# Optimization experiments

Measured on AMD Instinct MI355X. Metric: run time of the kernel, lower is better.

The kernel has to match this reference:

```python
import jax, jax.numpy as jnp
import numpy as np


def group_norm(x, g, b, groups, eps=1e-5):
    # x: (B, C, H, W), PyTorch GroupNorm semantics
    B, C, H, W = x.shape
    xr = x.reshape(B, groups, -1)
    m = xr.mean(-1, keepdims=True)
    v = xr.var(-1, keepdims=True)
    xn = ((xr - m) * jax.lax.rsqrt(v + eps)).reshape(B, C, H, W)
    return xn * g[:, None, None] + b[:, None, None]


def mamba(xs, in_w, conv_w, conv_b, xproj_w, dt_w, dt_b, A_log, D, out_w):
    # Standard Mamba block: in_proj -> causal depthwise conv -> SiLU ->
    # x_proj -> softplus(dt_proj) -> selective scan -> gate -> out_proj.
    Bsz, L, d = xs.shape
    di = in_w.shape[0] // 2
    r = dt_w.shape[1]
    n = A_log.shape[1]
    K = conv_w.shape[1]
    xz = xs @ in_w.T                           # (B, L, 2*di)
    xpart, z = xz[..., :di], xz[..., di:]
    xp = jnp.pad(xpart, ((0, 0), (K - 1, 0), (0, 0)))  # causal pad
    xc = conv_b + sum(xp[:, k:k + L, :] * conv_w[:, k] for k in range(K))
    xc = jax.nn.silu(xc)
    proj = xc @ xproj_w.T                      # (B, L, r + 2n)
    dt = proj[..., :r]
    Bm = proj[..., r:r + n]
    Cm = proj[..., r + n:]
    delta = jax.nn.softplus(dt @ dt_w.T + dt_b)   # (B, L, di)
    A = -jnp.exp(A_log)                            # (di, n)
    dA = jnp.exp(jnp.einsum('bld,dn->bldn', delta, A))
    dBu = jnp.einsum('bld,bln,bld->bldn', delta, Bm, xc)

    def step(h, inp):
        dA_t, dBu_t, C_t = inp
        h = dA_t * h + dBu_t                  # (B, di, n)
        return h, jnp.einsum('bdn,bn->bd', h, C_t)

    h0 = jnp.zeros((Bsz, di, n), xs.dtype)
    _, ys = jax.lax.scan(step, h0, (jnp.moveaxis(dA, 1, 0), jnp.moveaxis(dBu, 1, 0), jnp.moveaxis(Cm, 1, 0)))
    y = jnp.moveaxis(ys, 0, 1) + D * xc
    y = y * jax.nn.silu(z)
    return y @ out_w.T


def setup_inputs() -> dict:
    def nrm(i, shape, s=0.05):
        return jax.random.normal(jax.random.fold_in(jax.random.key(0), i), shape, dtype=jnp.float32) * s

    f32 = jnp.float32
    C = 128
    di, r, n = 256, 8, 16          # spa mamba: d_model=128, expand=2
    di2, r2 = 64, 2                # spe mamba: d_model=32
    A1 = jnp.log(jnp.broadcast_to(jnp.arange(1, n + 1, dtype=f32), (di, n)))
    A2 = jnp.log(jnp.broadcast_to(jnp.arange(1, n + 1, dtype=f32), (di2, n)))
    return {
        'x': nrm(0, (2, C, 64, 64), 1.0),
        'pe_w': nrm(1, (C, C)), 'pe_b': jnp.zeros((C,), f32),
        'pe_gn_g': jnp.ones((C,), f32), 'pe_gn_b': jnp.zeros((C,), f32),
        'spa_in_w': nrm(2, (2 * di, C)),
        'spa_conv_w': nrm(3, (di, 4)), 'spa_conv_b': jnp.zeros((di,), f32),
        'spa_xproj_w': nrm(4, (r + 2 * n, di)),
        'spa_dt_w': nrm(5, (di, r)), 'spa_dt_b': jnp.full((di,), -2.0, f32),
        'spa_Alog': A1, 'spa_D': jnp.ones((di,), f32),
        'spa_out_w': nrm(6, (C, di)),
        'spa_gn_g': jnp.ones((C,), f32), 'spa_gn_b': jnp.zeros((C,), f32),
        'spe_in_w': nrm(7, (2 * di2, 32)),
        'spe_conv_w': nrm(8, (di2, 4)), 'spe_conv_b': jnp.zeros((di2,), f32),
        'spe_xproj_w': nrm(9, (r2 + 2 * n, di2)),
        'spe_dt_w': nrm(10, (di2, r2)), 'spe_dt_b': jnp.full((di2,), -2.0, f32),
        'spe_Alog': A2, 'spe_D': jnp.ones((di2,), f32),
        'spe_out_w': nrm(11, (32, di2)),
        'spe_gn_g': jnp.ones((C,), f32), 'spe_gn_b': jnp.zeros((C,), f32),
        'fuse_w': jnp.full((2,), 0.5, f32),
        'cls_w': nrm(12, (10, C)), 'cls_b': jnp.zeros((10,), f32),
        'ref_dw_w': nrm(13, (C, 1, 3, 3)),
        'ref_gn_g': jnp.ones((C,), f32), 'ref_gn_b': jnp.zeros((C,), f32),
        'ref_pw_w': nrm(14, (1, C)), 'ref_pw_b': jnp.zeros((1,), f32),
        'alpha': jnp.asarray(1e-4, f32),
    }


def reference(x, pe_w, pe_b, pe_gn_g, pe_gn_b, spa_in_w, spa_conv_w, spa_conv_b, spa_xproj_w, spa_dt_w, spa_dt_b, spa_Alog, spa_D, spa_out_w, spa_gn_g, spa_gn_b, spe_in_w, spe_conv_w, spe_conv_b, spe_xproj_w, spe_dt_w, spe_dt_b, spe_Alog, spe_D, spe_out_w, spe_gn_g, spe_gn_b, fuse_w, cls_w, cls_b, ref_dw_w, ref_gn_g, ref_gn_b, ref_pw_w, ref_pw_b, alpha):
    B, _, H, W = x.shape
    # patch embedding: 1x1 conv + GroupNorm + SiLU
    h1 = jnp.einsum('bchw,oc->bohw', x, pe_w) + pe_b[:, None, None]
    h1 = jax.nn.silu(group_norm(h1, pe_gn_g, pe_gn_b, 4))
    # SpaMamba: scan over flattened spatial tokens (B, H*W, C)
    seq = h1.transpose(0, 2, 3, 1).reshape(B, H * W, -1)
    y = mamba(seq, spa_in_w, spa_conv_w, spa_conv_b, spa_xproj_w, spa_dt_w, spa_dt_b, spa_Alog, spa_D, spa_out_w)
    y = y.reshape(B, H, W, -1).transpose(0, 3, 1, 2)
    spa = jax.nn.silu(group_norm(y, spa_gn_g, spa_gn_b, 4)) + h1
    # SpeMamba: token_num=4, group_channel_num=32, channel_num=128 (no pad)
    seq2 = h1.transpose(0, 2, 3, 1).reshape(B * H * W, 4, 32)
    y2 = mamba(seq2, spe_in_w, spe_conv_w, spe_conv_b, spe_xproj_w, spe_dt_w, spe_dt_b, spe_Alog, spe_D, spe_out_w)
    y2 = y2.reshape(B, H, W, -1).transpose(0, 3, 1, 2)
    spe = h1 + jax.nn.silu(group_norm(y2, spe_gn_g, spe_gn_b, 4))
    # attention-weighted fusion + residual (BothMamba, use_att=True)
    wts = jax.nn.softmax(fuse_w)
    feat = spa * wts[0] + spe * wts[1] + h1
    # classifier head (1x1 conv)
    logits = jnp.einsum('bchw,oc->bohw', feat, cls_w) + cls_b[:, None, None]
    # BoundaryAwareLogitRefiner
    edge = jax.lax.conv_general_dilated(feat, ref_dw_w, (1, 1), ((1, 1), (1, 1)), feature_group_count=feat.shape[1], dimension_numbers=('NCHW', 'OIHW', 'NCHW'))
    edge = jax.nn.silu(group_norm(edge, ref_gn_g, ref_gn_b, 4))
    edge = jax.nn.sigmoid(jnp.einsum('bchw,oc->bohw', edge, ref_pw_w) + ref_pw_b[:, None, None])
    local = jax.lax.reduce_window(logits, 0.0, jax.lax.add, (1, 1, 3, 3), (1, 1, 1, 1), ((0, 0), (0, 0), (1, 1), (1, 1))) / 9.0  # count_include_pad=True
    return logits + alpha * (1.0 - edge) * (local - logits)
```

## Files before the change

### kernel.cpp

```cpp
#include <hip/hip_runtime.h>
#include <math.h>

#define DEV __device__ __forceinline__

DEV float sigm(float x){ return 1.f/(1.f+__expf(-x)); }
DEV float siluf(float x){ return x * sigm(x); }
DEV float softplusf(float x){ return x > 20.f ? x : log1pf(__expf(x)); }

static constexpr float NG = 131072.0f;
static constexpr float LOG2E = 1.4426950408889634f;

static constexpr size_t WS_H1    = 0;
static constexpr size_t WS_H1PRE = 1048576;
static constexpr size_t WS_XC    = 2097152;
static constexpr size_t WS_ZSIL  = 4194304;
static constexpr size_t WS_XZ    = 6291456;
static constexpr size_t WS_QOFF  = 6619136;
static constexpr size_t WS_LOG   = 8650752;
static constexpr size_t WS_Y     = 10485760;
static constexpr size_t WS_POFF  = 12582912;
static constexpr size_t WS_Y2    = 14155776;
static constexpr size_t WS_FEAT  = 15204352;
static constexpr size_t WS_STATS = 16252928;

__global__ void __launch_bounds__(256)
k_red(const float* __restrict__ part, float* __restrict__ outS, int half){
  __shared__ float red[4];
  int b = blockIdx.x >> 3, j = blockIdx.x & 7;
  float s = 0.f;
  for (int i = b*half + threadIdx.x; i < (b+1)*half; i += 256)
    s += part[(size_t)i*8 + j];
  s += __shfl_xor(s,1); s += __shfl_xor(s,2); s += __shfl_xor(s,4);
  s += __shfl_xor(s,8); s += __shfl_xor(s,16); s += __shfl_xor(s,32);
  if ((threadIdx.x & 63) == 0) red[threadIdx.x>>6] = s;
  __syncthreads();
  if (threadIdx.x == 0) outS[b*8+j] = red[0]+red[1]+red[2]+red[3];
}

__global__ void __launch_bounds__(256)
k_pe(const float* __restrict__ x, const float* __restrict__ pe_w,
     const float* __restrict__ pe_b, float* __restrict__ h1pre,
     float* __restrict__ part){
  __shared__ float As[16][36];
  __shared__ float Bs[16][64];
  __shared__ float red1[2][4], red2[2][4];
  int tid = threadIdx.x;
  int nx = blockIdx.x, my = blockIdx.y;
  int m0 = my*32, n0 = nx*64;
  int b = m0 >> 12, pl0 = m0 & 4095;
  int tx = tid & 15, ty = tid >> 4;
  float acc[2][4];
  #pragma unroll
  for (int i = 0; i < 2; i++)
    #pragma unroll
    for (int j = 0; j < 4; j++) acc[i][j] = 0.f;
  for (int k0 = 0; k0 < 128; k0 += 16){
    if (tid < 128){
      int k = tid >> 3, mm = (tid & 7)*4;
      float4 a = *(const float4*)(x + ((size_t)b*128 + k0+k)*4096 + pl0 + mm);
      *(float4*)&As[k][mm] = a;
    }
    {
      int n = tid >> 2, kq = (tid & 3)*4;
      float4 a = *(const float4*)(pe_w + (size_t)(n0+n)*128 + k0 + kq);
      Bs[kq+0][n] = a.x; Bs[kq+1][n] = a.y; Bs[kq+2][n] = a.z; Bs[kq+3][n] = a.w;
// ... 21 lines not shown
  }
  s1 += __shfl_xor(s1,1);  s2 += __shfl_xor(s2,1);
  s1 += __shfl_xor(s1,2);  s2 += __shfl_xor(s2,2);
  s1 += __shfl_xor(s1,4);  s2 += __shfl_xor(s2,4);
  s1 += __shfl_xor(s1,16); s2 += __shfl_xor(s2,16);
  s1 += __shfl_xor(s1,32); s2 += __shfl_xor(s2,32);
  int lane = tid & 63, w = tid >> 6;
  if ((lane & 55) == 0){
    int gl = (lane >> 3) & 1;
    red1[gl][w] = s1; red2[gl][w] = s2;
  }
  __syncthreads();
  if (tid < 8){
    int gg = tid >> 1, which = tid & 1;
    int gl = gg - nx*2;
    float v = 0.f;
    if (gl == 0 || gl == 1){
      v = which ? (red2[gl][0]+red2[gl][1]+red2[gl][2]+red2[gl][3])
                : (red1[gl][0]+red1[gl][1]+red1[gl][2]+red1[gl][3]);
    }
    int pblk = b*256 + (my & 127)*2 + nx;
    part[(size_t)pblk*8 + tid] = v;
  }
}

__global__ void __launch_bounds__(256)
k_xz(const float* __restrict__ h1pre, const float* __restrict__ in_w,
     const float* __restrict__ stats, const float* __restrict__ gng,
     const float* __restrict__ gnb, float* __restrict__ h1,
     float* __restrict__ xz, float* __restrict__ zsil){
  __shared__ float As[16][68];
  __shared__ float Bs[16][64];
  int tid = threadIdx.x;
  int m0 = blockIdx.y*64, n0 = blockIdx.x*64;
  int tx = tid & 15, ty = tid >> 4;
  float acc[4][4];
  #pragma unroll
  for (int i = 0; i < 4; i++)
    #pragma unroll
    for (int j = 0; j < 4; j++) acc[i][j] = 0.f;
  for (int k0 = 0; k0 < 128; k0 += 16){
    {
      int m = tid >> 2, kk = (tid & 3)*4;
      int pixm = m0 + m, c0 = k0 + kk;
      int bb = pixm >> 12, g = c0 >> 5;
      float4 a = *(const float4*)(h1pre + (size_t)pixm*128 + c0);
// ... 89 lines not shown
  {
    int t = tid & 15, jq = tid >> 4;
    int tok = m0 + t;
    float a0 = 0.f, a1 = 0.f, a2 = 0.f;
    for (int k0 = 0; k0 < 256; k0 += 4){
      float4 av = *(const float4*)&xct[t*260 + k0];
      float4 w0 = *(const float4*)(xpw + (size_t)jq*256 + k0);
      float4 w1 = *(const float4*)(xpw + (size_t)(jq+16)*256 + k0);
      a0 += av.x*w0.x + av.y*w0.y + av.z*w0.z + av.w*w0.w;
      a1 += av.x*w1.x + av.y*w1.y + av.z*w1.z + av.w*w1.w;
      if (jq < 8){
        float4 w2 = *(const float4*)(xpw + (size_t)(jq+32)*256 + k0);
        a2 += av.x*w2.x + av.y*w2.y + av.z*w2.z + av.w*w2.w;
      }
    }
    float* pr = proj + (size_t)tok*40;
    pr[jq] = a0;
    pr[jq+16] = a1;
    if (jq < 8) pr[jq+32] = a2;
  }
}

__global__ void __launch_bounds__(256)
k_delta(const float* __restrict__ proj, const float* __restrict__ dtw,
        const float* __restrict__ dtb, float* __restrict__ delta){
  int tid = threadIdx.x;
  int tok = blockIdx.x*4 + (tid >> 6);
  int lane = tid & 63;
  int d0 = lane*4;
  const float4* pr4 = (const float4*)(proj + (size_t)tok*40);
  float4 p0 = pr4[0], p1 = pr4[1];
  float4 outv;
  float* po = (float*)&outv;
  #pragma unroll
  for (int j = 0; j < 4; j++){
    int d = d0 + j;
    const float4* wr = (const float4*)(dtw + (size_t)d*8);
    float4 w0 = wr[0], w1 = wr[1];
    float v = dtb[d] + p0.x*w0.x + p0.y*w0.y + p0.z*w0.z + p0.w*w0.w
                     + p1.x*w1.x + p1.y*w1.y + p1.z*w1.z + p1.w*w1.w;
    po[j] = softplusf(v);
  }
  *(float4*)(delta + (size_t)tok*256 + d0) = outv;
}

__global__ void __launch_bounds__(256)
k_scan1(const float* __restrict__ delta, const float* __restrict__ proj,
        const float* __restrict__ xc, const float* __restrict__ Alog,
        float* __restrict__ P, float* __restrict__ Q){
  int blk = blockIdx.x;
  int dblk = blk & 3;
  int bc = blk >> 2;
  int b = bc >> 8, chunk = bc & 255;
  int tid = threadIdx.x;
  int dl = tid >> 2, ng = tid & 3;
  int d = dblk*64 + dl;
  float4 a4 = *(const float4*)(Alog + (size_t)d*16 + ng*4);
  float An[4] = {-__expf(a4.x)*LOG2E, -__expf(a4.y)*LOG2E,
                 -__expf(a4.z)*LOG2E, -__expf(a4.w)*LOG2E};
  float Pv[4] = {1.f,1.f,1.f,1.f}, Qv[4] = {0.f,0.f,0.f,0.f};
  size_t row0 = (size_t)(b*4096 + chunk*16);
  for (int l = 0; l < 16; l++){
    size_t r = row0 + l;
    float dv = delta[r*256 + d];
    float xv = xc[r*256 + d];
    float4 bm = *(const float4*)(proj + r*40 + 8 + ng*4);
    float dBx = dv*xv;
    float bmv[4] = {bm.x, bm.y, bm.z, bm.w};
    #pragma unroll
    for (int k = 0; k < 4; k++){
      float a = exp2f(dv*An[k]);
      Qv[k] = a*Qv[k] + bmv[k]*dBx;
      Pv[k] *= a;
    }
  }
  size_t o = (size_t)bc*4096 + dblk*1024 + tid*4;
  float4 pv; pv.x=Pv[0]; pv.y=Pv[1]; pv.z=Pv[2]; pv.w=Pv[3];
  float4 qv; qv.x=Qv[0]; qv.y=Qv[1]; qv.z=Qv[2]; qv.w=Qv[3];
  *(float4*)(P + o) = pv;
  *(float4*)(Q + o) = qv;
}

__global__ void __launch_bounds__(256)
k_scan2(const float* __restrict__ P, const float* __restrict__ Q,
        float* __restrict__ hs){
  __shared__ float Ps[256][17], Qs[256][17];
  int tid = threadIdx.x;
// ... 26 lines not shown
      if (lane >= off){ q = p*qp + q; p = p*pp; }
    }
    float h0 = __shfl_up(q, 1);
    if (lane == 0) h0 = 0.f;
    float h1 = p0*h0 + q0;
    float h2 = p1*h1 + q1;
    float h3 = p2*h2 + q2;
    Ps[4*lane+0][c] = h0;
    Ps[4*lane+1][c] = h1;
    Ps[4*lane+2][c] = h2;
    Ps[4*lane+3][c] = h3;
  }
  __syncthreads();
  for (int i = tid; i < 1024; i += 256){
    int ch = i >> 2, g = (i & 3)*4;
    size_t gaddr = (size_t)(b*256+ch)*4096 + dn0 + g;
    float4 h;
    h.x = Ps[ch][g]; h.y = Ps[ch][g+1]; h.z = Ps[ch][g+2]; h.w = Ps[ch][g+3];
    *(float4*)(hs + gaddr) = h;
  }
}

__global__ void __launch_bounds__(256)
k_scan3(const float* __restrict__ delta, const float* __restrict__ proj,
        const float* __restrict__ xc, const float* __restrict__ zsil,
        const float* __restrict__ Alog, const float* __restrict__ Dv,
        const float* __restrict__ hs, float* __restrict__ y){
  int blk = blockIdx.x;
  int dblk = blk & 3;
  int bc = blk >> 2;
  int b = bc >> 8, chunk = bc & 255;
  int tid = threadIdx.x;
  int dl = tid >> 2, ng = tid & 3;
  int d = dblk*64 + dl;
  float4 a4 = *(const float4*)(Alog + (size_t)d*16 + ng*4);
  float An[4] = {-__expf(a4.x)*LOG2E, -__expf(a4.y)*LOG2E,
                 -__expf(a4.z)*LOG2E, -__expf(a4.w)*LOG2E};
  float Dd = Dv[d];
  float h[4];
  {
    size_t o = (size_t)bc*4096 + dblk*1024 + tid*4;
    float4 hv = *(const float4*)(hs + o);
    h[0]=hv.x; h[1]=hv.y; h[2]=hv.z; h[3]=hv.w;
  }
  size_t row0 = (size_t)(b*4096 + chunk*16);
  for (int l = 0; l < 16; l++){
    size_t r = row0 + l;
    float dv = delta[r*256 + d];
    float xv = xc[r*256 + d];
    float4 bm = *(const float4*)(proj + r*40 + 8 + ng*4);
    float4 cm = *(const float4*)(proj + r*40 + 24 + ng*4);
    float dBx = dv*xv;
    float bmv[4] = {bm.x, bm.y, bm.z, bm.w};
    float cmv[4] = {cm.x, cm.y, cm.z, cm.w};
    float ys = 0.f;
    #pragma unroll
    for (int k = 0; k < 4; k++){
      float a = exp2f(dv*An[k]);
      h[k] = a*h[k] + bmv[k]*dBx;
      ys += h[k]*cmv[k];
    }
    ys += __shfl_xor(ys, 1);
    ys += __shfl_xor(ys, 2);
    if (ng == 0){
      float zv = zsil[r*256 + d];
      y[r*256 + d] = (ys + Dd*xv) * zv;
    }
  }
}

__global__ void __launch_bounds__(256)
k_outproj(const float* __restrict__ y, const float* __restrict__ out_w,
          float* __restrict__ yproj, float* __restrict__ part){
  __shared__ float As[16][36];
  __shared__ float Bs[16][64];
  __shared__ float red1[2][4], red2[2][4];
  int tid = threadIdx.x;
  int nx = blockIdx.x, my = blockIdx.y;
  int m0 = my*32, n0 = nx*64;
  int b = m0 >> 12;
  int tx = tid & 15, ty = tid >> 4;
  float acc[2][4];
  #pragma unroll
  for (int i = 0; i < 2; i++)
    #pragma unroll
    for (int j = 0; j < 4; j++) acc[i][j] = 0.f;
  for (int k0 = 0; k0 < 256; k0 += 16){
    if (tid < 128){
      int m = tid >> 2, kk = (tid & 3)*4;
      float4 a = *(const float4*)(y + (size_t)(m0+m)*256 + k0+kk);
      As[kk+0][m] = a.x; As[kk+1][m] = a.y; As[kk+2][m] = a.z; As[kk+3][m] = a.w;
    }
    {
      int n = tid >> 2, kq = (tid & 3)*4;
      float4 a = *(const float4*)(out_w + (size_t)(n0+n)*256 + k0 + kq);
      Bs[kq+0][n] = a.x; Bs[kq+1][n] = a.y; Bs[kq+2][n] = a.z; Bs[kq+3][n] = a.w;
// ... 18 lines not shown
  }
  s1 += __shfl_xor(s1,1);  s2 += __shfl_xor(s2,1);
  s1 += __shfl_xor(s1,2);  s2 += __shfl_xor(s2,2);
  s1 += __shfl_xor(s1,4);  s2 += __shfl_xor(s2,4);
  s1 += __shfl_xor(s1,16); s2 += __shfl_xor(s2,16);
  s1 += __shfl_xor(s1,32); s2 += __shfl_xor(s2,32);
  int lane = tid & 63, w = tid >> 6;
  if ((lane & 55) == 0){
    int gl = (lane >> 3) & 1;
    red1[gl][w] = s1; red2[gl][w] = s2;
  }
  __syncthreads();
  if (tid < 8){
    int gg = tid >> 1, which = tid & 1;
    int gl = gg - nx*2;
    float v = 0.f;
    if (gl == 0 || gl == 1){
      v = which ? (red2[gl][0]+red2[gl][1]+red2[gl][2]+red2[gl][3])
                : (red1[gl][0]+red1[gl][1]+red1[gl][2]+red1[gl][3]);
    }
    int pblk = b*256 + (my & 127)*2 + nx;
    part[(size_t)pblk*8 + tid] = v;
  }
}

__global__ void __launch_bounds__(256)
k_spe_a(const float* __restrict__ h1, const float* __restrict__ in_w,
        const float* __restrict__ conv_w, const float* __restrict__ conv_b,
        float* __restrict__ xc2, float* __restrict__ xc2T,
        float* __restrict__ zsil2){
  __shared__ float s_in[4][128];
  int tid = threadIdx.x;
  int w = tid >> 6, lane = tid & 63;
  float wx[32], wz[32];
  {
    const float4* rx = (const float4*)(in_w + (size_t)lane*32);
    const float4* rz = (const float4*)(in_w + (size_t)(64+lane)*32);
    #pragma unroll
    for (int k = 0; k < 8; k++){
      float4 a = rx[k]; wx[k*4]=a.x; wx[k*4+1]=a.y; wx[k*4+2]=a.z; wx[k*4+3]=a.w;
      float4 b = rz[k]; wz[k*4]=b.x; wz[k*4+1]=b.y; wz[k*4+2]=b.z; wz[k*4+3]=b.w;
    }
  }
  float4 cwv = ((const float4*)conv_w)[lane];
  float cbv = conv_b[lane];
  for (int i = 0; i < 4; i++){
    int pix = blockIdx.x*16 + w*4 + i;
    float2 hv = ((const float2*)(h1 + (size_t)pix*128))[lane];
    s_in[w][2*lane] = hv.x; s_in[w][2*lane+1] = hv.y;
    float xpr[4], zs[4];
    #pragma unroll
    for (int l = 0; l < 4; l++){
      const float4* sv = (const float4*)&s_in[w][l*32];
      float ax = 0.f, az = 0.f;
      #pragma unroll
      for (int c4 = 0; c4 < 8; c4++){
        float4 v = sv[c4];
        ax += v.x*wx[c4*4] + v.y*wx[c4*4+1] + v.z*wx[c4*4+2] + v.w*wx[c4*4+3];
        az += v.x*wz[c4*4] + v.y*wz[c4*4+1] + v.z*wz[c4*4+2] + v.w*wz[c4*4+3];
      }
      xpr[l] = ax; zs[l] = siluf(az);
    }
    #pragma unroll
    for (int l = 0; l < 4; l++){
      float v = cbv;
      if (l >= 3) v += xpr[l-3]*cwv.x;
      if (l >= 2) v += xpr[l-2]*cwv.y;
      if (l >= 1) v += xpr[l-1]*cwv.z;
      v += xpr[l]*cwv.w;
      float sx = siluf(v);
      int tok = pix*4 + l;
      xc2 [(size_t)tok*64 + lane] = sx;
      xc2T[(size_t)lane*32768 + tok] = sx;
      zsil2[(size_t)tok*64 + lane] = zs[l];
    }
  }
}

__global__ void __launch_bounds__(256)
k_spe_b(const float* __restrict__ xc2T, const float* __restrict__ xpw,
        float* __restrict__ proj){
  int tok = blockIdx.x*256 + threadIdx.x;
  float xcv[64];
  #pragma unroll 64
  for (int dd = 0; dd < 64; dd++) xcv[dd] = xc2T[(size_t)dd*32768 + tok];
  float* pr = proj + (size_t)tok*36;
  #pragma unroll 2
  for (int j = 0; j < 34; j++){
    const float4* wr = (const float4*)(xpw + j*64);
    float a = 0.f;
    #pragma unroll
    for (int k = 0; k < 16; k++){
      float4 wv = wr[k];
      a += xcv[k*4]*wv.x + xcv[k*4+1]*wv.y + xcv[k*4+2]*wv.z + xcv[k*4+3]*wv.w;
    }
    pr[j] = a;
  }
}

__global__ void __launch_bounds__(256)
k_spe_c(const float* __restrict__ xc2, const float* __restrict__ zsil2,
        const float* __restrict__ proj, const float* __restrict__ dt_w,
        const float* __restrict__ dt_b, const float* __restrict__ Alog,
        const float* __restrict__ Dvec, float* __restrict__ yg){
  int tid = threadIdx.x;
  int w = tid >> 6, lane = tid & 63;
  float2 dtwv = ((const float2*)dt_w)[lane];
  float dbv = dt_b[lane], Dd = Dvec[lane];
  float An[16];
  {
    const float4* ar = (const float4*)(Alog + (size_t)lane*16);
    #pragma unroll
    for (int k = 0; k < 4; k++){
      float4 a = ar[k];
      An[k*4]   = -__expf(a.x)*LOG2E; An[k*4+1] = -__expf(a.y)*LOG2E;
      An[k*4+2] = -__expf(a.z)*LOG2E; An[k*4+3] = -__expf(a.w)*LOG2E;
    }
  }
  for (int i = 0; i < 4; i++){
    int pix = blockIdx.x*16 + w*4 + i;
    float h[16];
    #pragma unroll
    for (int n = 0; n < 16; n++) h[n] = 0.f;
    #pragma unroll
    for (int l = 0; l < 4; l++){
      int tok = pix*4 + l;
      float pj[36];
      {
        const float4* pr = (const float4*)(proj + (size_t)tok*36);
        #pragma unroll
        for (int k = 0; k < 9; k++){
          float4 v = pr[k];
          pj[k*4]=v.x; pj[k*4+1]=v.y; pj[k*4+2]=v.z; pj[k*4+3]=v.w;
        }
      }
      float xv = xc2[(size_t)tok*64 + lane];
      float zv = zsil2[(size_t)tok*64 + lane];
      float dt = softplusf(dbv + pj[0]*dtwv.x + pj[1]*dtwv.y);
      float ys = 0.f;
      #pragma unroll
      for (int n = 0; n < 16; n++){
        float a = exp2f(dt * An[n]);
        h[n] = a*h[n] + dt * pj[2+n] * xv;
        ys += h[n] * pj[18+n];
      }
      yg[(size_t)tok*64 + lane] = (ys + Dd*xv) * zv;
    }
  }
}

__global__ void __launch_bounds__(256)
k_spe_d(const float* __restrict__ yg, const float* __restrict__ out_w,
        float* __restrict__ y2, float* __restrict__ part){
  __shared__ float ldsWT[64*32];
  __shared__ float bst[8];
  int tid = threadIdx.x;
  for (int i = tid; i < 2048; i += 256){
    int c2 = i >> 6, dd = i & 63;
    ldsWT[dd*32 + c2] = out_w[i];
  }
  if (tid < 8) bst[tid] = 0.f;
  __syncthreads();
  int w = tid >> 6, lane = tid & 63;
  int c2 = lane & 31, slot = lane >> 5;
  int tokbase = blockIdx.x*64 + w*16 + slot;
  float acc[8];
  #pragma unroll
  for (int i = 0; i < 8; i++) acc[i] = 0.f;
  for (int dd4 = 0; dd4 < 16; dd4++){
    float w0 = ldsWT[(dd4*4+0)*32 + c2];
    float w1 = ldsWT[(dd4*4+1)*32 + c2];
    float w2 = ldsWT[(dd4*4+2)*32 + c2];
    float w3 = ldsWT[(dd4*4+3)*32 + c2];
    #pragma unroll
    for (int i = 0; i < 8; i++){
      int tok = tokbase + 2*i;
      float4 yv = ((const float4*)(yg + (size_t)tok*64))[dd4];
      acc[i] += yv.x*w0 + yv.y*w1 + yv.z*w2 + yv.w*w3;
    }
  }
  #pragma unroll
  for (int i = 0; i < 8; i++){
    int tok = tokbase + 2*i;
    int pix = tok >> 2, l = tok & 3;
    y2[(size_t)pix*128 + l*32 + c2] = acc[i];
    float s1 = acc[i], s2 = acc[i]*acc[i];
    s1 += __shfl_xor(s1,1);  s2 += __shfl_xor(s2,1);
    s1 += __shfl_xor(s1,2);  s2 += __shfl_xor(s2,2);
    s1 += __shfl_xor(s1,4);  s2 += __shfl_xor(s2,4);
    s1 += __shfl_xor(s1,8);  s2 += __shfl_xor(s2,8);
    s1 += __shfl_xor(s1,16); s2 += __shfl_xor(s2,16);
    if (c2 == 0){
      atomicAdd(&bst[l*2+0], s1);
      atomicAdd(&bst[l*2+1], s2);
    }
  }
  __syncthreads();
  if (tid < 8) part[(size_t)blockIdx.x*8 + tid] = bst[tid];
}

__global__ void __launch_bounds__(256)
k_fuse(const float* __restrict__ h1, const float* __restrict__ yproj,
       const float* __restrict__ y2, const float* __restrict__ stats,
       const float* __restrict__ spa_g, const float* __restrict__ spa_b,
       const float* __restrict__ spe_g, const float* __restrict__ spe_b,
       const float* __restrict__ fuse_w, const float* __restrict__ cls_w,
       const float* __restrict__ cls_b, float* __restrict__ feat,
       float* __restrict__ logits){
  __shared__ float ft[2][128];
  int tid = threadIdx.x;
  int pixl = tid >> 7, c = tid & 127;
  int pix = blockIdx.x*2 + pixl;
  int b = pix >> 12, g = c >> 5;
  float m1 = stats[16 + (b*4+g)*2]   * (1.f/NG);
  float v1 = stats[16 + (b*4+g)*2+1] * (1.f/NG) - m1*m1;
  float m2 = stats[32 + (b*4+g)*2]   * (1.f/NG);
  float v2 = stats[32 + (b*4+g)*2+1] * (1.f/NG) - m2*m2;
  float h = h1[(size_t)pix*128 + c];
  float sa = siluf((yproj[(size_t)pix*128+c] - m1)*rsqrtf(v1+1e-5f)*spa_g[c] + spa_b[c]) + h;
  float sp = h + siluf((y2[(size_t)pix*128+c] - m2)*rsqrtf(v2+1e-5f)*spe_g[c] + spe_b[c]);
  float e0 = __expf(fuse_w[0]), e1 = __expf(fuse_w[1]);
  float w0 = e0/(e0+e1), w1 = e1/(e0+e1);
  float f = sa*w0 + sp*w1 + h;
  feat[(size_t)pix*128+c] = f;
  ft[pixl][c] = f;
  __syncthreads();
  if (tid < 20){
    int pl = (tid >= 10) ? 1 : 0;
    int o = tid - pl*10;
    float acc = cls_b[o];
    for (int cc = 0; cc < 128; cc++) acc += ft[pl][cc]*cls_w[o*128+cc];
    logits[(size_t)(blockIdx.x*2 + pl)*16 + o] = acc;
  }
}

__global__ void __launch_bounds__(256)
k_dw(const float* __restrict__ feat, const float* __restrict__ dww,
     float* __restrict__ epre, float* __restrict__ part){
  __shared__ float ft[100*128];
  __shared__ float red1[4][64], red2[4][64];
  int tid = threadIdx.x;
  int blk = blockIdx.x;
  int b = blk >> 6, ty = (blk >> 3) & 7, tx = blk & 7;
  for (int idx = tid; idx < 100*128; idx += 256){
    int row = idx >> 7, c = idx & 127;
    int r10 = row / 10, c10 = row - r10*10;
    int ry = ty*8 + r10 - 1, rx = tx*8 + c10 - 1;
    float v = 0.f;
    if (ry >= 0 && ry < 64 && rx >= 0 && rx < 64)
      v = feat[(size_t)((b<<12)|(ry<<6)|rx)*128 + c];
    ft[idx] = v;
  }
  __syncthreads();
  int c = tid & 127, pl = tid >> 7;
  float w[9];
  #pragma unroll
  for (int k = 0; k < 9; k++) w[k] = dww[c*9+k];
  float s1 = 0.f, s2 = 0.f;
  for (int i = 0; i < 32; i++){
    int pixl = i*2 + pl;
    int py = pixl >> 3, px = pixl & 7;
    float acc = 0.f;
    #pragma unroll
    for (int dy = 0; dy < 3; dy++)
      #pragma unroll
      for (int dx = 0; dx < 3; dx++)
        acc += ft[((py+dy)*10 + (px+dx))*128 + c] * w[dy*3+dx];
    epre[(size_t)((b<<12)|((ty*8+py)<<6)|(tx*8+px))*128 + c] = acc;
    s1 += acc; s2 += acc*acc;
  }
  int g = c >> 5;
  int idx = (c & 31) | (pl << 5);
  red1[g][idx] = s1; red2[g][idx] = s2;
  __syncthreads();
  int rg = tid >> 6, ridx = tid & 63;
  for (int s = 32; s >= 1; s >>= 1){
    if (ridx < s){ red1[rg][ridx] += red1[rg][ridx+s]; red2[rg][ridx] += red2[rg][ridx+s]; }
    __syncthreads();
  }
  if (ridx == 0){
    part[(size_t)blk*8 + rg*2+0] = red1[rg][0];
    part[(size_t)blk*8 + rg*2+1] = red2[rg][0];
  }
}

__global__ void __launch_bounds__(256)
k_final(const float* __restrict__ epre, const float* __restrict__ logits,
        const float* __restrict__ stats, const float* __restrict__ rg_g,
        const float* __restrict__ rg_b, const float* __restrict__ pw_w,
        const float* __restrict__ pw_b, const float* __restrict__ alpha,
        float* __restrict__ outp){
  __shared__ float part[4];
  __shared__ float edge_s[2];
  int tid = threadIdx.x;
  int pixl = tid >> 7, c = tid & 127;
  int pix = blockIdx.x*2 + pixl;
  int b = pix >> 12, p = pix & 4095, yy = p >> 6, xx = p & 63;
  int g = c >> 5;
  float m = stats[48 + (b*4+g)*2]   * (1.f/NG);
  float v = stats[48 + (b*4+g)*2+1] * (1.f/NG) - m*m;
  float e = epre[(size_t)pix*128+c];
  float en = siluf((e-m)*rsqrtf(v+1e-5f)*rg_g[c] + rg_b[c]);
  float pv = en * pw_w[c];
  pv += __shfl_xor(pv,1);  pv += __shfl_xor(pv,2);  pv += __shfl_xor(pv,4);
  pv += __shfl_xor(pv,8);  pv += __shfl_xor(pv,16); pv += __shfl_xor(pv,32);
  if ((tid & 63) == 0) part[tid>>6] = pv;
// ... 42 lines not shown
  const float* spe_xproj_w= (const float*)d_in[19];
  const float* spe_dt_w   = (const float*)d_in[20];
  const float* spe_dt_b   = (const float*)d_in[21];
  const float* spe_Alog   = (const float*)d_in[22];
  const float* spe_D      = (const float*)d_in[23];
  const float* spe_out_w  = (const float*)d_in[24];
  const float* spe_gn_g   = (const float*)d_in[25];
  const float* spe_gn_b   = (const float*)d_in[26];
  const float* fuse_w     = (const float*)d_in[27];
  const float* cls_w      = (const float*)d_in[28];
  const float* cls_b      = (const float*)d_in[29];
  const float* ref_dw_w   = (const float*)d_in[30];
  const float* ref_gn_g   = (const float*)d_in[31];
  const float* ref_gn_b   = (const float*)d_in[32];
  const float* ref_pw_w   = (const float*)d_in[33];
  const float* ref_pw_b   = (const float*)d_in[34];
  const float* alpha      = (const float*)d_in[35];
  float* ws  = (float*)d_ws;
  float* out = (float*)d_out;

  float* Pb    = ws + WS_POFF;
  float* Qb    = ws + WS_QOFF;
  float* HSb   = Pb;
  float* dely  = ws + WS_Y;
  float* partPE  = ws + WS_Y;
  float* partSPA = ws + WS_POFF;
  float* partSPE = ws + WS_POFF + 16384;
  float* partDW  = ws + WS_POFF + 65536;
  float* proj  = ws + WS_FEAT;
  float* xc2   = ws + WS_XC;
  float* xc2T  = ws + WS_ZSIL;
  float* zsil2 = ws + WS_XZ;
  float* proj2 = ws + WS_XZ + 2097152;
  float* yg    = ws + WS_Y;

  k_pe<<<dim3(2,256),256,0,stream>>>(x, pe_w, pe_b, ws+WS_H1PRE, partPE);
  k_red<<<16,256,0,stream>>>(partPE, ws+WS_STATS+0, 256);
  k_xz<<<dim3(8,128),256,0,stream>>>(ws+WS_H1PRE, spa_in_w, ws+WS_STATS,
      pe_gn_g, pe_gn_b, ws+WS_H1, ws+WS_XZ, ws+WS_ZSIL);
  k_projc<<<512,256,0,stream>>>(ws+WS_XZ, spa_conv_w, spa_conv_b, spa_xproj_w,
      ws+WS_XC, proj);
  k_delta<<<2048,256,0,stream>>>(proj, spa_dt_w, spa_dt_b, dely);
  k_scan1<<<2048,256,0,stream>>>(dely, proj, ws+WS_XC, spa_Alog, Pb, Qb);
  k_scan2<<<512,256,0,stream>>>(Pb, Qb, HSb);
  k_scan3<<<2048,256,0,stream>>>(dely, proj, ws+WS_XC, ws+WS_ZSIL,
      spa_Alog, spa_D, HSb, dely);
  k_outproj<<<dim3(2,256),256,0,stream>>>(dely, spa_out_w, ws+WS_H1PRE, partSPA);
  k_red<<<16,256,0,stream>>>(partSPA, ws+WS_STATS+16, 256);
  k_spe_a<<<512,256,0,stream>>>(ws+WS_H1, spe_in_w, spe_conv_w, spe_conv_b,
      xc2, xc2T, zsil2);
  k_spe_b<<<128,256,0,stream>>>(xc2T, spe_xproj_w, proj2);
  k_spe_c<<<512,256,0,stream>>>(xc2, zsil2, proj2, spe_dt_w, spe_dt_b,
      spe_Alog, spe_D, yg);
  k_spe_d<<<512,256,0,stream>>>(yg, spe_out_w, ws+WS_Y2, partSPE);
  k_red<<<16,256,0,stream>>>(partSPE, ws+WS_STATS+32, 256);
  k_fuse<<<4096,256,0,stream>>>(ws+WS_H1, ws+WS_H1PRE, ws+WS_Y2, ws+WS_STATS,
      spa_gn_g, spa_gn_b, spe_gn_g, spe_gn_b, fuse_w, cls_w, cls_b,
      ws+WS_FEAT, ws+WS_LOG);
  k_dw<<<128,256,0,stream>>>(ws+WS_FEAT, ref_dw_w, ws+WS_Y, partDW);
  k_red<<<16,256,0,stream>>>(partDW, ws+WS_STATS+48, 64);
  k_final<<<4096,256,0,stream>>>(ws+WS_Y, ws+WS_LOG, ws+WS_STATS,
      ref_gn_g, ref_gn_b, ref_pw_w, ref_pw_b, alpha, out);
  (void)in_sizes; (void)n_in; (void)out_size; (void)ws_size;
}
```

Before: 384.1 us.

## Fuse stat reductions via last-block, inline delta into scans, merge spectral Mamba kernels

Replaces the separate k_red launches with a last-block-done reduction using an atomic counter in each stats-producing kernel. It also folds the dt projection and softplus into scan1/scan3 instead of materialising delta. The four spectral Mamba kernels become one kernel that keeps xc, proj and y in LDS. This cuts kernel launches and global round-trips of intermediates, at the cost of recomputing delta in both scan passes, more LDS per block, and an extra memset plus atomic fences.

Measured after the change: 529.0 us. 1.38x slower.

```diff
diff --git a/kernel.cpp b/kernel.cpp
--- a/kernel.cpp
+++ b/kernel.cpp
@@ -22,25 +22,33 @@
 static constexpr size_t WS_Y2    = 14155776;
 static constexpr size_t WS_FEAT  = 15204352;
 static constexpr size_t WS_STATS = 16252928;
-
-__global__ void __launch_bounds__(256)
-k_red(const float* __restrict__ part, float* __restrict__ outS, int half){
-  __shared__ float red[4];
-  int b = blockIdx.x >> 3, j = blockIdx.x & 7;
+static constexpr size_t WS_CNT   = 16252992;
+
+DEV void stats_lastblock(const float* part, int rowsPerB, int gridBlocks,
+                         int* cnt, float* statsOut){
+  __shared__ int lastS;
+  int tid = threadIdx.x;
+  __threadfence();
+  __syncthreads();
+  if (tid == 0) lastS = (atomicAdd(cnt, 1) == gridBlocks - 1) ? 1 : 0;
+  __syncthreads();
+  if (!lastS) return;
+  __threadfence();
+  int p = tid >> 4, sl = tid & 15;
+  int b = p >> 3, j = p & 7;
   float s = 0.f;
-  for (int i = b*half + threadIdx.x; i < (b+1)*half; i += 256)
-    s += part[(size_t)i*8 + j];
-  s += __shfl_xor(s,1); s += __shfl_xor(s,2); s += __shfl_xor(s,4);
-  s += __shfl_xor(s,8); s += __shfl_xor(s,16); s += __shfl_xor(s,32);
-  if ((threadIdx.x & 63) == 0) red[threadIdx.x>>6] = s;
-  __syncthreads();
-  if (threadIdx.x == 0) outS[b*8+j] = red[0]+red[1]+red[2]+red[3];
+  volatile const float* vp = (volatile const float*)part;
+  for (int row = sl; row < rowsPerB; row += 16)
+    s += vp[((size_t)b*rowsPerB + row)*8 + j];
+  s += __shfl_xor(s,1); s += __shfl_xor(s,2);
+  s += __shfl_xor(s,4); s += __shfl_xor(s,8);
+  if (sl == 0) statsOut[p] = s;
 }
 
 __global__ void __launch_bounds__(256)
 k_pe(const float* __restrict__ x, const float* __restrict__ pe_w,
      const float* __restrict__ pe_b, float* __restrict__ h1pre,
-     float* __restrict__ part){
+     float* __restrict__ part, int* __restrict__ cnt, float* __restrict__ statsOut){
   __shared__ float As[16][36];
   __shared__ float Bs[16][64];
   __shared__ float red1[2][4], red2[2][4];
@@ -108,6 +116,7 @@
     int pblk = b*256 + (my & 127)*2 + nx;
     part[(size_t)pblk*8 + tid] = v;
   }
+  stats_lastblock(part, 256, 512, cnt, statsOut);
 }
 
 __global__ void __launch_bounds__(256)
@@ -243,32 +252,10 @@
 }
 
 __global__ void __launch_bounds__(256)
-k_delta(const float* __restrict__ proj, const float* __restrict__ dtw,
-        const float* __restrict__ dtb, float* __restrict__ delta){
-  int tid = threadIdx.x;
-  int tok = blockIdx.x*4 + (tid >> 6);
-  int lane = tid & 63;
-  int d0 = lane*4;
-  const float4* pr4 = (const float4*)(proj + (size_t)tok*40);
-  float4 p0 = pr4[0], p1 = pr4[1];
-  float4 outv;
-  float* po = (float*)&outv;
-  #pragma unroll
-  for (int j = 0; j < 4; j++){
-    int d = d0 + j;
-    const float4* wr = (const float4*)(dtw + (size_t)d*8);
-    float4 w0 = wr[0], w1 = wr[1];
-    float v = dtb[d] + p0.x*w0.x + p0.y*w0.y + p0.z*w0.z + p0.w*w0.w
-                     + p1.x*w1.x + p1.y*w1.y + p1.z*w1.z + p1.w*w1.w;
-    po[j] = softplusf(v);
-  }
-  *(float4*)(delta + (size_t)tok*256 + d0) = outv;
-}
-
-__global__ void __launch_bounds__(256)
-k_scan1(const float* __restrict__ delta, const float* __restrict__ proj,
-        const float* __restrict__ xc, const float* __restrict__ Alog,
-        float* __restrict__ P, float* __restrict__ Q){
+k_scan1(const float* __restrict__ proj, const float* __restrict__ xc,
+        const float* __restrict__ dtw, const float* __restrict__ dtb,
+        const float* __restrict__ Alog, float* __restrict__ P,
+        float* __restrict__ Q){
   int blk = blockIdx.x;
   int dblk = blk & 3;
   int bc = blk >> 2;
@@ -279,11 +266,17 @@
   float4 a4 = *(const float4*)(Alog + (size_t)d*16 + ng*4);
   float An[4] = {-__expf(a4.x)*LOG2E, -__expf(a4.y)*LOG2E,
                  -__expf(a4.z)*LOG2E, -__expf(a4.w)*LOG2E};
+  const float4* wr = (const float4*)(dtw + (size_t)d*8);
+  float4 w0 = wr[0], w1 = wr[1];
+  float bd = dtb[d];
   float Pv[4] = {1.f,1.f,1.f,1.f}, Qv[4] = {0.f,0.f,0.f,0.f};
   size_t row0 = (size_t)(b*4096 + chunk*16);
   for (int l = 0; l < 16; l++){
     size_t r = row0 + l;
-    float dv = delta[r*256 + d];
+    const float4* pr4 = (const float4*)(proj + r*40);
+    float4 p0 = pr4[0], p1 = pr4[1];
+    float dv = softplusf(bd + p0.x*w0.x + p0.y*w0.y + p0.z*w0.z + p0.w*w0.w
+                            + p1.x*w1.x + p1.y*w1.y + p1.z*w1.z + p1.w*w1.w);
     float xv = xc[r*256 + d];
     float4 bm = *(const float4*)(proj + r*40 + 8 + ng*4);
     float dBx = dv*xv;
@@ -356,10 +349,11 @@
 }
 
 __global__ void __launch_bounds__(256)
-k_scan3(const float* __restrict__ delta, const float* __restrict__ proj,
-        const float* __restrict__ xc, const float* __restrict__ zsil,
-        const float* __restrict__ Alog, const float* __restrict__ Dv,
-        const float* __restrict__ hs, float* __restrict__ y){
+k_scan3(const float* __restrict__ proj, const float* __restrict__ xc,
+        const float* __restrict__ zsil, const float* __restrict__ dtw,
+        const float* __restrict__ dtb, const float* __restrict__ Alog,
+        const float* __restrict__ Dv, const float* __restrict__ hs,
+        float* __restrict__ y){
   int blk = blockIdx.x;
   int dblk = blk & 3;
   int bc = blk >> 2;
@@ -370,6 +364,9 @@
   float4 a4 = *(const float4*)(Alog + (size_t)d*16 + ng*4);
   float An[4] = {-__expf(a4.x)*LOG2E, -__expf(a4.y)*LOG2E,
                  -__expf(a4.z)*LOG2E, -__expf(a4.w)*LOG2E};
+  const float4* wr = (const float4*)(dtw + (size_t)d*8);
+  float4 w0 = wr[0], w1 = wr[1];
+  float bd = dtb[d];
   float Dd = Dv[d];
   float h[4];
   {
@@ -380,7 +377,10 @@
   size_t row0 = (size_t)(b*4096 + chunk*16);
   for (int l = 0; l < 16; l++){
     size_t r = row0 + l;
-    float dv = delta[r*256 + d];
+    const float4* pr4 = (const float4*)(proj + r*40);
+    float4 p0 = pr4[0], p1 = pr4[1];
+    float dv = softplusf(bd + p0.x*w0.x + p0.y*w0.y + p0.z*w0.z + p0.w*w0.w
+                            + p1.x*w1.x + p1.y*w1.y + p1.z*w1.z + p1.w*w1.w);
     float xv = xc[r*256 + d];
     float4 bm = *(const float4*)(proj + r*40 + 8 + ng*4);
     float4 cm = *(const float4*)(proj + r*40 + 24 + ng*4);
@@ -405,7 +405,8 @@
 
 __global__ void __launch_bounds__(256)
 k_outproj(const float* __restrict__ y, const float* __restrict__ out_w,
-          float* __restrict__ yproj, float* __restrict__ part){
+          float* __restrict__ yproj, float* __restrict__ part,
+          int* __restrict__ cnt, float* __restrict__ statsOut){
   __shared__ float As[16][36];
   __shared__ float Bs[16][64];
   __shared__ float red1[2][4], red2[2][4];
@@ -470,18 +471,27 @@
     int pblk = b*256 + (my & 127)*2 + nx;
     part[(size_t)pblk*8 + tid] = v;
   }
-}
-
-__global__ void __launch_bounds__(256)
-k_spe_a(const float* __restrict__ h1, const float* __restrict__ in_w,
-        const float* __restrict__ conv_w, const float* __restrict__ conv_b,
-        float* __restrict__ xc2, float* __restrict__ xc2T,
-        float* __restrict__ zsil2){
+  stats_lastblock(part, 256, 512, cnt, statsOut);
+}
+
+__global__ void __launch_bounds__(256)
+k_spe(const float* __restrict__ h1, const float* __restrict__ in_w,
+      const float* __restrict__ conv_w, const float* __restrict__ conv_b,
+      const float* __restrict__ xpw, const float* __restrict__ dt_w,
+      const float* __restrict__ dt_b, const float* __restrict__ Alog,
+      const float* __restrict__ Dvec, const float* __restrict__ out_w,
+      float* __restrict__ y2, float* __restrict__ part,
+      int* __restrict__ cnt, float* __restrict__ statsOut){
+  __shared__ float s_xc[64][66];
+  __shared__ float s_pr[64][37];
   __shared__ float s_in[4][128];
+  __shared__ float bst[8];
   int tid = threadIdx.x;
   int w = tid >> 6, lane = tid & 63;
-  float wx[32], wz[32];
+  if (tid < 8) bst[tid] = 0.f;
+  float xcr[4][4], zsr[4][4];
   {
+    float wx[32], wz[32];
     const float4* rx = (const float4*)(in_w + (size_t)lane*32);
     const float4* rz = (const float4*)(in_w + (size_t)(64+lane)*32);
     #pragma unroll
@@ -489,74 +499,64 @@
       float4 a = rx[k]; wx[k*4]=a.x; wx[k*4+1]=a.y; wx[k*4+2]=a.z; wx[k*4+3]=a.w;
       float4 b = rz[k]; wz[k*4]=b.x; wz[k*4+1]=b.y; wz[k*4+2]=b.z; wz[k*4+3]=b.w;
     }
-  }
-  float4 cwv = ((const float4*)conv_w)[lane];
-  float cbv = conv_b[lane];
-  for (int i = 0; i < 4; i++){
-    int pix = blockIdx.x*16 + w*4 + i;
-    float2 hv = ((const float2*)(h1 + (size_t)pix*128))[lane];
-    s_in[w][2*lane] = hv.x; s_in[w][2*lane+1] = hv.y;
-    float xpr[4], zs[4];
-    #pragma unroll
-    for (int l = 0; l < 4; l++){
-      const float4* sv = (const float4*)&s_in[w][l*32];
-      float ax = 0.f, az = 0.f;
+    float4 cwv = ((const float4*)conv_w)[lane];
+    float cbv = conv_b[lane];
+    #pragma unroll
+    for (int i = 0; i < 4; i++){
+      int pix = blockIdx.x*16 + w*4 + i;
+      float2 hv = ((const float2*)(h1 + (size_t)pix*128))[lane];
+      s_in[w][2*lane] = hv.x; s_in[w][2*lane+1] = hv.y;
+      float xpr[4];
       #pragma unroll
-      for (int c4 = 0; c4 < 8; c4++){
-        float4 v = sv[c4];
-        ax += v.x*wx[c4*4] + v.y*wx[c4*4+1] + v.z*wx[c4*4+2] + v.w*wx[c4*4+3];
-        az += v.x*wz[c4*4] + v.y*wz[c4*4+1] + v.z*wz[c4*4+2] + v.w*wz[c4*4+3];
+      for (int l = 0; l < 4; l++){
+        const float4* sv = (const float4*)&s_in[w][l*32];
+        float ax = 0.f, az = 0.f;
+        #pragma unroll
+        for (int c4 = 0; c4 < 8; c4++){
+          float4 v = sv[c4];
+          ax += v.x*wx[c4*4] + v.y*wx[c4*4+1] + v.z*wx[c4*4+2] + v.w*wx[c4*4+3];
+          az += v.x*wz[c4*4] + v.y*wz[c4*4+1] + v.z*wz[c4*4+2] + v.w*wz[c4*4+3];
+        }
+        xpr[l] = ax; zsr[i][l] = siluf(az);
       }
-      xpr[l] = ax; zs[l] = siluf(az);
-    }
-    #pragma unroll
-    for (int l = 0; l < 4; l++){
-      float v = cbv;
-      if (l >= 3) v += xpr[l-3]*cwv.x;
-      if (l >= 2) v += xpr[l-2]*cwv.y;
-      if (l >= 1) v += xpr[l-1]*cwv.z;
-      v += xpr[l]*cwv.w;
-      float sx = siluf(v);
-      int tok = pix*4 + l;
-      xc2 [(size_t)tok*64 + lane] = sx;
-      xc2T[(size_t)lane*32768 + tok] = sx;
-      zsil2[(size_t)tok*64 + lane] = zs[l];
-    }
-  }
-}
-
-__global__ void __launch_bounds__(256)
-k_spe_b(const float* __restrict__ xc2T, const float* __restrict__ xpw,
-        float* __restrict__ proj){
-  int tok = blockIdx.x*256 + threadIdx.x;
-  float xcv[64];
-  #pragma unroll 64
-  for (int dd = 0; dd < 64; dd++) xcv[dd] = xc2T[(size_t)dd*32768 + tok];
-  float* pr = proj + (size_t)tok*36;
-  #pragma unroll 2
-  for (int j = 0; j < 34; j++){
-    const float4* wr = (const float4*)(xpw + j*64);
-    float a = 0.f;
-    #pragma unroll
-    for (int k = 0; k < 16; k++){
-      float4 wv = wr[k];
-      a += xcv[k*4]*wv.x + xcv[k*4+1]*wv.y + xcv[k*4+2]*wv.z + xcv[k*4+3]*wv.w;
-    }
-    pr[j] = a;
-  }
-}
-
-__global__ void __launch_bounds__(256)
-k_spe_c(const float* __restrict__ xc2, const float* __restrict__ zsil2,
-        const float* __restrict__ proj, const float* __restrict__ dt_w,
-        const float* __restrict__ dt_b, const float* __restrict__ Alog,
-        const float* __restrict__ Dvec, float* __restrict__ yg){
-  int tid = threadIdx.x;
-  int w = tid >> 6, lane = tid & 63;
-  float2 dtwv = ((const float2*)dt_w)[lane];
-  float dbv = dt_b[lane], Dd = Dvec[lane];
-  float An[16];
+      #pragma unroll
+      for (int l = 0; l < 4; l++){
+        float v = cbv;
+        if (l >= 3) v += xpr[l-3]*cwv.x;
+        if (l >= 2) v += xpr[l-2]*cwv.y;
+        if (l >= 1) v += xpr[l-1]*cwv.z;
+        v += xpr[l]*cwv.w;
+        float sx = siluf(v);
+        xcr[i][l] = sx;
+        s_xc[(w*4+i)*4 + l][lane] = sx;
+      }
+    }
+  }
+  __syncthreads();
   {
+    int t = lane;
+    float a[9];
+    #pragma unroll
+    for (int j = 0; j < 9; j++) a[j] = 0.f;
+    for (int k = 0; k < 64; k++){
+      float xk = s_xc[t][k];
+      #pragma unroll
+      for (int j = 0; j < 9; j++){
+        int ja = w*9 + j; if (ja > 33) ja = 33;
+        a[j] += xk * xpw[(size_t)ja*64 + k];
+      }
+    }
+    #pragma unroll
+    for (int j = 0; j < 9; j++){
+      int ja = w*9 + j;
+      if (ja < 34) s_pr[t][ja] = a[j];
+    }
+  }
+  __syncthreads();
+  {
+    float2 dtwv = ((const float2*)dt_w)[lane];
+    float dbv = dt_b[lane], Dd = Dvec[lane];
+    float An[16];
     const float4* ar = (const float4*)(Alog + (size_t)lane*16);
     #pragma unroll
     for (int k = 0; k < 4; k++){
@@ -564,87 +564,61 @@
       An[k*4]   = -__expf(a.x)*LOG2E; An[k*4+1] = -__expf(a.y)*LOG2E;
       An[k*4+2] = -__expf(a.z)*LOG2E; An[k*4+3] = -__expf(a.w)*LOG2E;
     }
-  }
-  for (int i = 0; i < 4; i++){
-    int pix = blockIdx.x*16 + w*4 + i;
-    float h[16];
-    #pragma unroll
-    for (int n = 0; n < 16; n++) h[n] = 0.f;
-    #pragma unroll
-    for (int l = 0; l < 4; l++){
-      int tok = pix*4 + l;
-      float pj[36];
-      {
-        const float4* pr = (const float4*)(proj + (size_t)tok*36);
+    #pragma unroll
+    for (int i = 0; i < 4; i++){
+      float h[16];
+      #pragma unroll
+      for (int n = 0; n < 16; n++) h[n] = 0.f;
+      #pragma unroll
+      for (int l = 0; l < 4; l++){
+        int t = (w*4+i)*4 + l;
+        float dt = softplusf(dbv + s_pr[t][0]*dtwv.x + s_pr[t][1]*dtwv.y);
+        float xv = xcr[i][l], zv = zsr[i][l];
+        float ys = 0.f;
         #pragma unroll
-        for (int k = 0; k < 9; k++){
-          float4 v = pr[k];
-          pj[k*4]=v.x; pj[k*4+1]=v.y; pj[k*4+2]=v.z; pj[k*4+3]=v.w;
+        for (int n = 0; n < 16; n++){
+          float a = exp2f(dt * An[n]);
+          h[n] = a*h[n] + dt * s_pr[t][2+n] * xv;
+          ys += h[n] * s_pr[t][18+n];
         }
+        s_xc[t][lane] = (ys + Dd*xv) * zv;
       }
-      float xv = xc2[(size_t)tok*64 + lane];
-      float zv = zsil2[(size_t)tok*64 + lane];
-      float dt = softplusf(dbv + pj[0]*dtwv.x + pj[1]*dtwv.y);
-      float ys = 0.f;
+    }
+  }
+  __syncthreads();
+  {
+    int t = lane, cg = w;
+    float acc[8];
+    #pragma unroll
+    for (int q = 0; q < 8; q++) acc[q] = 0.f;
+    for (int dd = 0; dd < 64; dd++){
+      float yv = s_xc[t][dd];
       #pragma unroll
-      for (int n = 0; n < 16; n++){
-        float a = exp2f(dt * An[n]);
-        h[n] = a*h[n] + dt * pj[2+n] * xv;
-        ys += h[n] * pj[18+n];
-      }
-      yg[(size_t)tok*64 + lane] = (ys + Dd*xv) * zv;
-    }
-  }
-}
-
-__global__ void __launch_bounds__(256)
-k_spe_d(const float* __restrict__ yg, const float* __restrict__ out_w,
-        float* __restrict__ y2, float* __restrict__ part){
-  __shared__ float ldsWT[64*32];
-  __shared__ float bst[8];
-  int tid = threadIdx.x;
-  for (int i = tid; i < 2048; i += 256){
-    int c2 = i >> 6, dd = i & 63;
-    ldsWT[dd*32 + c2] = out_w[i];
-  }
-  if (tid < 8) bst[tid] = 0.f;
-  __syncthreads();
-  int w = tid >> 6, lane = tid & 63;
-  int c2 = lane & 31, slot = lane >> 5;
-  int tokbase = blockIdx.x*64 + w*16 + slot;
-  float acc[8];
-  #pragma unroll
-  for (int i = 0; i < 8; i++) acc[i] = 0.f;
-  for (int dd4 = 0; dd4 < 16; dd4++){
-    float w0 = ldsWT[(dd4*4+0)*32 + c2];
-    float w1 = ldsWT[(dd4*4+1)*32 + c2];
-    float w2 = ldsWT[(dd4*4+2)*32 + c2];
-    float w3 = ldsWT[(dd4*4+3)*32 + c2];
-    #pragma unroll
-    for (int i = 0; i < 8; i++){
-      int tok = tokbase + 2*i;
-      float4 yv = ((const float4*)(yg + (size_t)tok*64))[dd4];
-      acc[i] += yv.x*w0 + yv.y*w1 + yv.z*w2 + yv.w*w3;
-    }
-  }
-  #pragma unroll
-  for (int i = 0; i < 8; i++){
-    int tok = tokbase + 2*i;
+      for (int q = 0; q < 8; q++)
+        acc[q] += yv * out_w[(size_t)(cg*8+q)*64 + dd];
+    }
+    int tok = blockIdx.x*64 + t;
     int pix = tok >> 2, l = tok & 3;
-    y2[(size_t)pix*128 + l*32 + c2] = acc[i];
-    float s1 = acc[i], s2 = acc[i]*acc[i];
-    s1 += __shfl_xor(s1,1);  s2 += __shfl_xor(s2,1);
-    s1 += __shfl_xor(s1,2);  s2 += __shfl_xor(s2,2);
+    float4 o0, o1;
+    o0.x=acc[0]; o0.y=acc[1]; o0.z=acc[2]; o0.w=acc[3];
+    o1.x=acc[4]; o1.y=acc[5]; o1.z=acc[6]; o1.w=acc[7];
+    *(float4*)(y2 + (size_t)pix*128 + l*32 + cg*8)     = o0;
+    *(float4*)(y2 + (size_t)pix*128 + l*32 + cg*8 + 4) = o1;
+    float s1 = 0.f, s2 = 0.f;
+    #pragma unroll
+    for (int q = 0; q < 8; q++){ s1 += acc[q]; s2 += acc[q]*acc[q]; }
     s1 += __shfl_xor(s1,4);  s2 += __shfl_xor(s2,4);
     s1 += __shfl_xor(s1,8);  s2 += __shfl_xor(s2,8);
     s1 += __shfl_xor(s1,16); s2 += __shfl_xor(s2,16);
-    if (c2 == 0){
-      atomicAdd(&bst[l*2+0], s1);
-      atomicAdd(&bst[l*2+1], s2);
+    s1 += __shfl_xor(s1,32); s2 += __shfl_xor(s2,32);
+    if (lane < 4){
+      atomicAdd(&bst[lane*2+0], s1);
+      atomicAdd(&bst[lane*2+1], s2);
     }
   }
   __syncthreads();
   if (tid < 8) part[(size_t)blockIdx.x*8 + tid] = bst[tid];
+  stats_lastblock(part, 256, 512, cnt, statsOut);
 }
 
 __global__ void __launch_bounds__(256)
@@ -684,7 +658,8 @@
 
 __global__ void __launch_bounds__(256)
 k_dw(const float* __restrict__ feat, const float* __restrict__ dww,
-     float* __restrict__ epre, float* __restrict__ part){
+     float* __restrict__ epre, float* __restrict__ part,
+     int* __restrict__ cnt, float* __restrict__ statsOut){
   __shared__ float ft[100*128];
   __shared__ float red1[4][64], red2[4][64];
   int tid = threadIdx.x;
@@ -730,6 +705,7 @@
     part[(size_t)blk*8 + rg*2+0] = red1[rg][0];
     part[(size_t)blk*8 + rg*2+1] = red2[rg][0];
   }
+  stats_lastblock(part, 64, 128, cnt, statsOut);
 }
 
 __global__ void __launch_bounds__(256)
@@ -818,43 +794,35 @@
   float* Pb    = ws + WS_POFF;
   float* Qb    = ws + WS_QOFF;
   float* HSb   = Pb;
-  float* dely  = ws + WS_Y;
+  int*   cnt   = (int*)(ws + WS_CNT);
   float* partPE  = ws + WS_Y;
   float* partSPA = ws + WS_POFF;
   float* partSPE = ws + WS_POFF + 16384;
   float* partDW  = ws + WS_POFF + 65536;
   float* proj  = ws + WS_FEAT;
-  float* xc2   = ws + WS_XC;
-  float* xc2T  = ws + WS_ZSIL;
-  float* zsil2 = ws + WS_XZ;
-  float* proj2 = ws + WS_XZ + 2097152;
-  float* yg    = ws + WS_Y;
-
-  k_pe<<<dim3(2,256),256,0,stream>>>(x, pe_w, pe_b, ws+WS_H1PRE, partPE);
-  k_red<<<16,256,0,stream>>>(partPE, ws+WS_STATS+0, 256);
+
+  hipMemsetAsync(cnt, 0, 4*sizeof(int), stream);
+  k_pe<<<dim3(2,256),256,0,stream>>>(x, pe_w, pe_b, ws+WS_H1PRE, partPE,
+      cnt+0, ws+WS_STATS+0);
   k_xz<<<dim3(8,128),256,0,stream>>>(ws+WS_H1PRE, spa_in_w, ws+WS_STATS,
       pe_gn_g, pe_gn_b, ws+WS_H1, ws+WS_XZ, ws+WS_ZSIL);
   k_projc<<<512,256,0,stream>>>(ws+WS_XZ, spa_conv_w, spa_conv_b, spa_xproj_w,
       ws+WS_XC, proj);
-  k_delta<<<2048,256,0,stream>>>(proj, spa_dt_w, spa_dt_b, dely);
-  k_scan1<<<2048,256,0,stream>>>(dely, proj, ws+WS_XC, spa_Alog, Pb, Qb);
+  k_scan1<<<2048,256,0,stream>>>(proj, ws+WS_XC, spa_dt_w, spa_dt_b, spa_Alog,
+      Pb, Qb);
   k_scan2<<<512,256,0,stream>>>(Pb, Qb, HSb);
-  k_scan3<<<2048,256,0,stream>>>(dely, proj, ws+WS_XC, ws+WS_ZSIL,
-      spa_Alog, spa_D, HSb, dely);
-  k_outproj<<<dim3(2,256),256,0,stream>>>(dely, spa_out_w, ws+WS_H1PRE, partSPA);
-  k_red<<<16,256,0,stream>>>(partSPA, ws+WS_STATS+16, 256);
-  k_spe_a<<<512,256,0,stream>>>(ws+WS_H1, spe_in_w, spe_conv_w, spe_conv_b,
-      xc2, xc2T, zsil2);
-  k_spe_b<<<128,256,0,stream>>>(xc2T, spe_xproj_w, proj2);
-  k_spe_c<<<512,256,0,stream>>>(xc2, zsil2, proj2, spe_dt_w, spe_dt_b,
-      spe_Alog, spe_D, yg);
-  k_spe_d<<<512,256,0,stream>>>(yg, spe_out_w, ws+WS_Y2, partSPE);
-  k_red<<<16,256,0,stream>>>(partSPE, ws+WS_STATS+32, 256);
+  k_scan3<<<2048,256,0,stream>>>(proj, ws+WS_XC, ws+WS_ZSIL, spa_dt_w, spa_dt_b,
+      spa_Alog, spa_D, HSb, ws+WS_Y);
+  k_outproj<<<dim3(2,256),256,0,stream>>>(ws+WS_Y, spa_out_w, ws+WS_H1PRE,
+      partSPA, cnt+1, ws+WS_STATS+16);
+  k_spe<<<512,256,0,stream>>>(ws+WS_H1, spe_in_w, spe_conv_w, spe_conv_b,
+      spe_xproj_w, spe_dt_w, spe_dt_b, spe_Alog, spe_D, spe_out_w,
+      ws+WS_Y2, partSPE, cnt+2, ws+WS_STATS+32);
   k_fuse<<<4096,256,0,stream>>>(ws+WS_H1, ws+WS_H1PRE, ws+WS_Y2, ws+WS_STATS,
       spa_gn_g, spa_gn_b, spe_gn_g, spe_gn_b, fuse_w, cls_w, cls_b,
       ws+WS_FEAT, ws+WS_LOG);
-  k_dw<<<128,256,0,stream>>>(ws+WS_FEAT, ref_dw_w, ws+WS_Y, partDW);
-  k_red<<<16,256,0,stream>>>(partDW, ws+WS_STATS+48, 64);
+  k_dw<<<128,256,0,stream>>>(ws+WS_FEAT, ref_dw_w, ws+WS_Y, partDW,
+      cnt+3, ws+WS_STATS+48);
   k_final<<<4096,256,0,stream>>>(ws+WS_Y, ws+WS_LOG, ws+WS_STATS,
       ref_gn_g, ref_gn_b, ref_pw_w, ref_pw_b, alpha, out);
   (void)in_sizes; (void)n_in; (void)out_size; (void)ws_size;
```
